# Kernel tuning notes

Measured on AMD Instinct MI355X. Metric: run time of the kernel, lower is better.

## Reference

```python
import jax, jax.numpy as jnp
import numpy as np

B, S, D = 1, 2048, 4096
HQ, HK, HD = 32, 8, 128


def setup_inputs() -> dict:
    key = jax.random.key(0)
    ks = jax.random.split(key, 6)
    x = jax.random.normal(ks[0], (B, S, D), jnp.float32) * 0.02
    wq = jax.random.normal(ks[1], (D, HQ * HD), jnp.float32) * 0.02
    wk = jax.random.normal(ks[2], (D, HK * HD), jnp.float32) * 0.02
    wv = jax.random.normal(ks[3], (D, HK * HD), jnp.float32) * 0.02
    wo = jax.random.normal(ks[4], (HQ * HD, D), jnp.float32) * 0.02
    # canonical RoPE frequencies: theta = 10000
    inv_freq = 1.0 / (10000.0 ** (jnp.arange(0, HD, 2, dtype=jnp.float32) / HD))  # [HD/2]
    t = jnp.arange(S, dtype=jnp.float32)
    ang = jnp.outer(t, inv_freq)  # [S, HD/2]
    return {
        "x": x,
        "freqs_cos": jnp.cos(ang),
        "freqs_sin": jnp.sin(ang),
        "wq": wq, "wk": wk, "wv": wv, "wo": wo,
    }


def _rope(t, cos, sin):
    # t: [B, S, H, HD]; pairs are consecutive elements (view_as_complex semantics)
    tr = t.reshape(*t.shape[:-1], HD // 2, 2)
    t0, t1 = tr[..., 0], tr[..., 1]
    c = cos[None, :, None, :]
    s = sin[None, :, None, :]
    o0 = t0 * c - t1 * s
    o1 = t0 * s + t1 * c
    return jnp.stack([o0, o1], axis=-1).reshape(t.shape)


def reference(x, freqs_cos, freqs_sin, wq, wk, wv, wo):
    b, s, _ = x.shape
    g = HQ // HK  # GQA group size
    xq = (x @ wq).reshape(b, s, HQ, HD)
    xk = (x @ wk).reshape(b, s, HK, HD)
    xv = (x @ wv).reshape(b, s, HK, HD)
    xq = _rope(xq, freqs_cos, freqs_sin)
    xk = _rope(xk, freqs_cos, freqs_sin)
    scale = 1.0 / jnp.sqrt(jnp.float32(HD))
    xqg = xq.reshape(b, s, HK, g, HD)
    # scores: [b, HK, g, s_q, s_k]
    scores = jnp.einsum("bqkgd,bnkd->bkgqn", xqg, xk) * scale
    causal = jnp.tril(jnp.ones((s, s), dtype=bool))
    scores = jnp.where(causal[None, None, None, :, :], scores, -jnp.inf)
    p = jax.nn.softmax(scores, axis=-1)
    out = jnp.einsum("bkgqn,bnkd->bqkgd", p, xv).reshape(b, s, HQ * HD)
    return out @ wo
```

## Files before the change

kernel.cpp:

```cpp
#include <hip/hip_runtime.h>
#include <stdint.h>

typedef __bf16 bf16_t;
typedef bf16_t bf16x8 __attribute__((ext_vector_type(8)));
typedef float f32x4 __attribute__((ext_vector_type(4)));
typedef unsigned int u32;
typedef unsigned short u16;

#define DEV_INLINE __device__ __forceinline__

#define S_LEN 2048
#define D_MODEL 4096
#define HQ 32
#define HK 8
#define HD 128
#define NQKV 6144

DEV_INLINE u16 f2bf(float x) {
  union { float f; uint32_t u; } v; v.f = x;
  uint32_t r = v.u + 0x7FFFu + ((v.u >> 16) & 1u);
  return (u16)(r >> 16);
}
DEV_INLINE float bf2f(u16 x) {
  union { uint32_t u; float f; } v; v.u = ((uint32_t)x) << 16;
  return v.f;
}
DEV_INLINE u32 pack2bf(float a, float b) {
  return (u32)f2bf(a) | ((u32)f2bf(b) << 16);
}

DEV_INLINE void async_load16(const void* g, void* l) {
  __builtin_amdgcn_global_load_lds(
      (const __attribute__((address_space(1))) u32*)g,
      (__attribute__((address_space(3))) u32*)l, 16, 0, 0);
}

DEV_INLINE f32x4 mfma16(bf16x8 a, bf16x8 b, f32x4 c) {
  return __builtin_amdgcn_mfma_f32_16x16x32_bf16(a, b, c, 0, 0, 0);
}

__global__ void cvt_f32_bf16(const float* __restrict__ in, u16* __restrict__ out, int n) {
  int i = (blockIdx.x * blockDim.x + threadIdx.x) * 4;
  if (i >= n) return;
  float4 v = *(const float4*)(in + i);
  union { u16 s[4]; uint2 u; } o;
  o.s[0] = f2bf(v.x); o.s[1] = f2bf(v.y); o.s[2] = f2bf(v.z); o.s[3] = f2bf(v.w);
  *(uint2*)(out + i) = o.u;
}

__global__ void transpose_f32_bf16(const float* __restrict__ in, u16* __restrict__ out,
                                   int R, int C) {
  __shared__ float tile[64][65];
  int tx = threadIdx.x, ty = threadIdx.y;
  int c0 = blockIdx.x * 64, r0 = blockIdx.y * 64;
#pragma unroll
  for (int i = 0; i < 16; ++i)
    tile[ty + i * 4][tx] = in[(long)(r0 + ty + i * 4) * C + c0 + tx];
  __syncthreads();
#pragma unroll
  for (int i = 0; i < 16; ++i)
    out[(long)(c0 + ty + i * 4) * R + r0 + tx] = f2bf(tile[tx][ty + i * 4]);
}

__global__ void transpose_bf16(const u16* __restrict__ in, u16* __restrict__ out,
                               int R, int C, int ld_in, int col_off) {
  __shared__ u16 tile[32][33];
  int tx = threadIdx.x, ty = threadIdx.y;
  int c0 = blockIdx.x * 32, r0 = blockIdx.y * 32;
#pragma unroll
  for (int i = 0; i < 4; ++i)
    tile[ty + i * 8][tx] = in[(long)(r0 + ty + i * 8) * ld_in + col_off + c0 + tx];
  __syncthreads();
#pragma unroll
  for (int i = 0; i < 4; ++i)
    out[(long)(c0 + ty + i * 8) * R + r0 + tx] = tile[tx][ty + i * 8];
}

__global__ void rope_bf16(const u16* __restrict__ in, const float* __restrict__ cosb,
                          const float* __restrict__ sinb, u16* __restrict__ out,
                          int H, int ld_in, int col_off, float scale) {
  int idx = blockIdx.x * blockDim.x + threadIdx.x;
  int j = idx & 63;
  int sh = idx >> 6;
  int s = sh / H, h = sh - s * H;
  const u16* ip = in + (long)s * ld_in + col_off + h * HD;
  union { u32 u; u16 s2[2]; } v; v.u = *(const u32*)(ip + 2 * j);
  float q0 = bf2f(v.s2[0]), q1 = bf2f(v.s2[1]);
  float c = cosb[s * 64 + j], sn = sinb[s * 64 + j];
  union { u16 s2[2]; u32 u; } o;
  o.s2[0] = f2bf((q0 * c - q1 * sn) * scale);
  o.s2[1] = f2bf((q0 * sn + q1 * c) * scale);
  *(u32*)(out + (long)sh * HD + 2 * j) = o.u;
}

#define BARRIER() asm volatile("s_barrier" ::: "memory")
#define WAIT_VM(N) asm volatile("s_waitcnt vmcnt(" #N ")" ::: "memory")

template <int BN, bool BF16OUT>
__global__ __launch_bounds__(256, 2) void gemm_db(
    const u16* __restrict__ A, const u16* __restrict__ Bt, void* __restrict__ Cv,
    int N, int K) {
  constexpr int NF = BN / 64;
  constexpr int BPT = (BN * 4) / 256;
  constexpr int LDSU = (128 + BN) * 32;

  __shared__ __attribute__((aligned(16))) u16 lds[2][LDSU];

  const int tid = threadIdx.x;
  const int lane = tid & 63, wave = tid >> 6;
  const int quad = lane >> 4, l15 = lane & 15;

  const int gx = gridDim.x;
  const int bid = blockIdx.y * gx + blockIdx.x;
  const int cpx = (gx * gridDim.y) >> 3;
  const int sw = (bid & 7) * cpx + (bid >> 3);
  const int bn = sw % gx, bm = sw / gx;

  const long arow = (long)bm * 128, brow = (long)bn * BN;
  const int NT = K >> 5;

  auto stage = [&](int ts) {
    const int k0 = ts * 32;
    u16* base = &lds[ts & 1][0];
#pragma unroll
    for (int j = 0; j < 2; ++j) {
      int c = tid + j * 256;
      int row = c >> 2, cc = c & 3, cs = cc ^ ((row >> 1) & 3);
      async_load16(A + (arow + row) * (long)K + k0 + cs * 8, base + c * 8);
    }
#pragma unroll
    for (int j = 0; j < BPT; ++j) {
      int c = tid + j * 256;
      int row = c >> 2, cc = c & 3, cs = cc ^ ((row >> 1) & 3);
      async_load16(Bt + (brow + row) * (long)K + k0 + cs * 8,
                   base + 4096 + c * 8);
    }
  };
  auto rdfrag = [&](const u16* base, int row) -> bf16x8 {
    return *(const bf16x8*)(base + row * 32 + ((quad ^ ((row >> 1) & 3)) * 8));
  };

  f32x4 acc[8][NF] = {};

  stage(0);
  WAIT_VM(0);
  BARRIER();

  for (int t = 0; t < NT; ++t) {
    if (t + 1 < NT) stage(t + 1);
    const u16* Ab = &lds[t & 1][0];
    const u16* Bb = Ab + 4096;
    bf16x8 bfr[NF];
#pragma unroll
    for (int j = 0; j < NF; ++j)
      bfr[j] = rdfrag(Bb, wave * (NF * 16) + j * 16 + l15);
    __builtin_amdgcn_s_setprio(1);
#pragma unroll
    for (int i = 0; i < 8; ++i) {
      bf16x8 af = rdfrag(Ab, i * 16 + l15);
#pragma unroll
      for (int j = 0; j < NF; ++j)
        acc[i][j] = mfma16(af, bfr[j], acc[i][j]);
    }
    __builtin_amdgcn_s_setprio(0);
    WAIT_VM(0);
    BARRIER();
  }

#pragma unroll
  for (int i = 0; i < 8; ++i) {
    const long row = (long)bm * 128 + i * 16 + quad * 4;
#pragma unroll
    for (int j = 0; j < NF; ++j) {
      const int col = bn * BN + wave * (NF * 16) + j * 16 + l15;
      if constexpr (BF16OUT) {
        u16* C = (u16*)Cv;
#pragma unroll
        for (int r = 0; r < 4; ++r) C[(row + r) * N + col] = f2bf(acc[i][j][r]);
      } else {
        float* C = (float*)Cv;
#pragma unroll
        for (int r = 0; r < 4; ++r) C[(row + r) * N + col] = acc[i][j][r];
      }
    }
  }
}

#define NEG_INF -1e30f
__global__ __launch_bounds__(256, 2) void attn_fwd(
    const u16* __restrict__ Qb, const u16* __restrict__ Kb,
    const u16* __restrict__ Vt, u16* __restrict__ Ob) {
  __shared__ __attribute__((aligned(16))) u16 Ks[2][64 * 128];
  __shared__ __attribute__((aligned(16))) u16 Vs[2][128 * 64];
  __shared__ __attribute__((aligned(16))) u16 Pts[4][16 * 64];
  const int tid = threadIdx.x;
  const int lane = tid & 63, wave = tid >> 6;
  const int quad = lane >> 4, l15 = lane & 15;
  const int lin = blockIdx.y * gridDim.x + blockIdx.x;
  const int h = lin & 31;
  const int pp = (lin >> 5) & 7;
  const int u = (lin >> 8) ? 15 - pp : pp;
  const int hk = h >> 2;
  const int swz = 2 * (l15 & 7);
  const int nt = 2 * (u + 1);

  bf16x8 qf[2][4];
#pragma unroll
  for (int n = 0; n < 2; ++n) {
    const u16* qrow = Qb + (long)(u * 128 + wave * 32 + n * 16 + l15) * (HQ * HD)
                      + h * HD + quad * 8;
#pragma unroll
    for (int ks = 0; ks < 4; ++ks) qf[n][ks] = *(const bf16x8*)(qrow + ks * 32);
  }

  auto stage = [&](int t) {
    const int b = t & 1;
#pragma unroll
    for (int it = 0; it < 4; ++it) {
      int c = tid + it * 256;
      int row = c >> 4, cc = c & 15, cs = cc ^ (row & 15);
      async_load16(Kb + (long)(t * 64 + row) * (HK * HD) + hk * HD + cs * 8,
                   (u16*)&Ks[b][0] + c * 8);
    }
#pragma unroll
    for (int it = 0; it < 4; ++it) {
      int c = tid + it * 256;
      int row = c >> 3, cc = c & 7, cs = cc ^ (row & 7);
      async_load16(Vt + (long)(hk * HD + row) * S_LEN + t * 64 + cs * 8,
                   (u16*)&Vs[b][0] + c * 8);
    }
  };

  float m_run[2] = {NEG_INF, NEG_INF}, l_run[2] = {0.f, 0.f};
  f32x4 oacc[8][2] = {};

  stage(0);
  __syncthreads();

  for (int t = 0; t < nt; ++t) {
    const int cur = t & 1;
    if (t + 1 < nt) stage(t + 1);

    if (t * 64 <= u * 128 + wave * 32 + 31) {
      f32x4 sc[4][2] = {};
      __builtin_amdgcn_s_setprio(1);
#pragma unroll
      for (int ks = 0; ks < 4; ++ks)
#pragma unroll
        for (int tj = 0; tj < 4; ++tj) {
          int row = tj * 16 + l15;
          bf16x8 kf = *(const bf16x8*)(&Ks[cur][0] + row * 128
                                       + (((ks * 4 + quad) ^ (row & 15)) * 8));
          sc[tj][0] = mfma16(kf, qf[0][ks], sc[tj][0]);
          sc[tj][1] = mfma16(kf, qf[1][ks], sc[tj][1]);
        }
      __builtin_amdgcn_s_setprio(0);

      const bool diag = (t >= 2 * u);
      const int kbase = t * 64 - u * 128;
#pragma unroll
      for (int n = 0; n < 2; ++n) {
        int qloc = wave * 32 + n * 16 + l15;
        if (diag) {
#pragma unroll
          for (int tj = 0; tj < 4; ++tj)
#pragma unroll
            for (int r = 0; r < 4; ++r)
              if (kbase + tj * 16 + quad * 4 + r > qloc) sc[tj][n][r] = NEG_INF;
        }
        float m = NEG_INF;
#pragma unroll
        for (int tj = 0; tj < 4; ++tj)
#pragma unroll
          for (int r = 0; r < 4; ++r) m = fmaxf(m, sc[tj][n][r]);
        m = fmaxf(m, __shfl_xor(m, 16));
        m = fmaxf(m, __shfl_xor(m, 32));
        if (!__all(m - m_run[n] <= 8.0f)) {
          float mnew = fmaxf(m_run[n], m);
          float alpha = __expf(m_run[n] - mnew);
          m_run[n] = mnew;
          l_run[n] *= alpha;
#pragma unroll
          for (int tj = 0; tj < 8; ++tj) oacc[tj][n] *= alpha;
        }
        float rs = 0.f;
#pragma unroll
        for (int tj = 0; tj < 4; ++tj)
#pragma unroll
          for (int r = 0; r < 4; ++r) {
            float p = __expf(sc[tj][n][r] - m_run[n]);
            sc[tj][n][r] = p;
            rs += p;
          }
        rs += __shfl_xor(rs, 16);
        rs += __shfl_xor(rs, 32);
        l_run[n] += rs;
      }

      u16* pw = &Pts[wave][0];
      bf16x8 pf0[2], pf1[2];
#pragma unroll
      for (int tj = 0; tj < 4; ++tj) {
        union { u32 w[2]; uint2 u2; } pk;
        pk.w[0] = pack2bf(sc[tj][0][0], sc[tj][0][1]);
        pk.w[1] = pack2bf(sc[tj][0][2], sc[tj][0][3]);
        *(uint2*)(pw + l15 * 64 + (((tj * 4 + quad) ^ swz) * 4)) = pk.u2;
      }
      __asm__ volatile("s_waitcnt lgkmcnt(0)" ::: "memory");
#pragma unroll
      for (int ks = 0; ks < 2; ++ks)
        pf0[ks] = *(const bf16x8*)(pw + l15 * 64 + (((ks * 8 + quad * 2) ^ swz) * 4));
      __asm__ volatile("s_waitcnt lgkmcnt(0)" ::: "memory");
#pragma unroll
      for (int tj = 0; tj < 4; ++tj) {
        union { u32 w[2]; uint2 u2; } pk;
        pk.w[0] = pack2bf(sc[tj][1][0], sc[tj][1][1]);
        pk.w[1] = pack2bf(sc[tj][1][2], sc[tj][1][3]);
        *(uint2*)(pw + l15 * 64 + (((tj * 4 + quad) ^ swz) * 4)) = pk.u2;
      }
      __asm__ volatile("s_waitcnt lgkmcnt(0)" ::: "memory");
#pragma unroll
      for (int ks = 0; ks < 2; ++ks)
        pf1[ks] = *(const bf16x8*)(pw + l15 * 64 + (((ks * 8 + quad * 2) ^ swz) * 4));

      __builtin_amdgcn_s_setprio(1);
#pragma unroll
      for (int ks = 0; ks < 2; ++ks)
#pragma unroll
        for (int tj = 0; tj < 8; ++tj) {
          int row = tj * 16 + l15;
          bf16x8 vf = *(const bf16x8*)(&Vs[cur][0] + row * 64
                                       + (((ks * 4 + quad) ^ (row & 7)) * 8));
          oacc[tj][0] = mfma16(vf, pf0[ks], oacc[tj][0]);
          oacc[tj][1] = mfma16(vf, pf1[ks], oacc[tj][1]);
        }
      __builtin_amdgcn_s_setprio(0);
    }

    __syncthreads();
  }

#pragma unroll
  for (int n = 0; n < 2; ++n) {
    float inv_l = 1.0f / l_run[n];
    long grow = u * 128 + wave * 32 + n * 16 + l15;
#pragma unroll
    for (int tj = 0; tj < 8; ++tj) {
      int gcol = h * HD + tj * 16 + quad * 4;
      union { u32 w[2]; uint2 u2; } pk;
      pk.w[0] = pack2bf(oacc[tj][n][0] * inv_l, oacc[tj][n][1] * inv_l);
      pk.w[1] = pack2bf(oacc[tj][n][2] * inv_l, oacc[tj][n][3] * inv_l);
      *(uint2*)(Ob + grow * (HQ * HD) + gcol) = pk.u2;
    }
  }
}

#define MB (1024L * 1024L)

extern "C" void kernel_launch(void* const* d_in, const int* in_sizes, int n_in,
                              void* d_out, int out_size, void* d_ws, size_t ws_size,
                              hipStream_t stream) {
  const float* x    = (const float*)d_in[0];
  const float* fcos = (const float*)d_in[1];
  const float* fsin = (const float*)d_in[2];
  const float* wq   = (const float*)d_in[3];
  const float* wk   = (const float*)d_in[4];
  const float* wv   = (const float*)d_in[5];
  const float* wo   = (const float*)d_in[6];
  float* out = (float*)d_out;

  char* ws = (char*)d_ws;
  u16* wt    = (u16*)(ws + 0 * MB);
  u16* xb    = (u16*)(ws + 48 * MB);
  u16* QKVb  = (u16*)(ws + 64 * MB);
  u16* Qb    = (u16*)(ws + 88 * MB);
  u16* Kb    = (u16*)(ws + 104 * MB);
  u16* Vt    = (u16*)(ws + 108 * MB);
  u16* attnb = (u16*)(ws + 112 * MB);

  const int M = S_LEN, D = D_MODEL;

  cvt_f32_bf16<<<(M * D) / 1024, 256, 0, stream>>>(x, xb, M * D);

  transpose_f32_bf16<<<dim3(D / 64, D / 64), dim3(64, 4), 0, stream>>>(wq, wt, D, HQ * HD);
  transpose_f32_bf16<<<dim3((HK * HD) / 64, D / 64), dim3(64, 4), 0, stream>>>(
      wk, wt + (long)(HQ * HD) * D, D, HK * HD);
  transpose_f32_bf16<<<dim3((HK * HD) / 64, D / 64), dim3(64, 4), 0, stream>>>(
      wv, wt + (long)(HQ * HD + HK * HD) * D, D, HK * HD);

  gemm_db<192, true><<<dim3(NQKV / 192, M / 128), 256, 0, stream>>>(
      xb, wt, QKVb, NQKV, D);

  rope_bf16<<<(M * HQ * 64) / 256, 256, 0, stream>>>(
      QKVb, fcos, fsin, Qb, HQ, NQKV, 0, 0.08838834764831845f);
  rope_bf16<<<(M * HK * 64) / 256, 256, 0, stream>>>(
      QKVb, fcos, fsin, Kb, HK, NQKV, HQ * HD, 1.0f);
  transpose_bf16<<<dim3((HK * HD) / 32, M / 32), dim3(32, 8), 0, stream>>>(
      QKVb, Vt, M, HK * HD, NQKV, HQ * HD + HK * HD);

  attn_fwd<<<dim3(16, HQ), 256, 0, stream>>>(Qb, Kb, Vt, attnb);

  transpose_f32_bf16<<<dim3(D / 64, D / 64), dim3(64, 4), 0, stream>>>(wo, wt, HQ * HD, D);
  gemm_db<128, false><<<dim3(D / 128, M / 128), 256, 0, stream>>>(
      attnb, wt, out, D, HQ * HD);
}
```

Measured before the change: 507.3 us.

## Replace double-buffered GEMM with 4-stage prefetching 512-thread GEMM

The GEMM becomes a 256-row tile computed by 512 threads in a 2D wave grid, with a 4-deep LDS ring buffer staged three tiles ahead. Register fragments are double-buffered so LDS reads for the next k-tile overlap the current MFMAs. The goal is to hide global-load latency and raise reuse per block. In exchange it needs much more LDS per block and more registers, and the fewer, larger blocks may reduce occupancy and tail balance.

```diff
diff --git a/kernel.cpp b/kernel.cpp
--- a/kernel.cpp
+++ b/kernel.cpp
@@ -96,19 +96,65 @@
 #define BARRIER() asm volatile("s_barrier" ::: "memory")
 #define WAIT_VM(N) asm volatile("s_waitcnt vmcnt(" #N ")" ::: "memory")
 
-template <int BN, bool BF16OUT>
-__global__ __launch_bounds__(256, 2) void gemm_db(
+#define VML() do { if constexpr (LPT == 4) { WAIT_VM(4); } else { WAIT_VM(3); } } while (0)
+
+#define KTILE(T, FAC, FAN, FBC, FBN, DO_READ, DO_STAGE, WMODE)            \
+  {                                                                       \
+    bf16x8 fbl[NF];                                                       \
+    if constexpr (!PFB) {                                                 \
+      const u16* Bb_ = &lds[(T) & 3][8192];                               \
+      _Pragma("unroll")                                                   \
+      for (int j = 0; j < NF; ++j)                                        \
+        fbl[j] = rdfrag(Bb_, wc * WCOLS + j * 16 + l15);                  \
+    }                                                                     \
+    if (DO_READ) {                                                        \
+      const u16* An_ = &lds[((T) + 1) & 3][0];                            \
+      _Pragma("unroll")                                                   \
+      for (int i = 0; i < MF; ++i)                                        \
+        FAN[i] = rdfrag(An_, wr * MROWS + i * 16 + l15);                  \
+      if constexpr (PFB) {                                                \
+        _Pragma("unroll")                                                 \
+        for (int j = 0; j < NF; ++j)                                      \
+          FBN[j] = rdfrag(An_ + 8192, wc * WCOLS + j * 16 + l15);         \
+      }                                                                   \
+    }                                                                     \
+    if (DO_STAGE) stageAB((T) + 3);                                       \
+    __builtin_amdgcn_s_setprio(1);                                        \
+    _Pragma("unroll")                                                     \
+    for (int i = 0; i < MF; ++i)                                          \
+      _Pragma("unroll")                                                   \
+      for (int j = 0; j < NF; ++j) {                                      \
+        if constexpr (PFB) acc[i][j] = mfma16(FAC[i], FBC[j], acc[i][j]); \
+        else               acc[i][j] = mfma16(FAC[i], fbl[j], acc[i][j]); \
+      }                                                                   \
+    __builtin_amdgcn_s_setprio(0);                                        \
+    if ((WMODE) == 0) { VML(); }                                          \
+    else if ((WMODE) == 1) { WAIT_VM(0); }                                \
+    BARRIER();                                                            \
+  }
+
+template <int BN, int WM, bool BF16OUT>
+__global__ __launch_bounds__(512, 2) void gemm_pf(
     const u16* __restrict__ A, const u16* __restrict__ Bt, void* __restrict__ Cv,
     int N, int K) {
-  constexpr int NF = BN / 64;
-  constexpr int BPT = (BN * 4) / 256;
-  constexpr int LDSU = (128 + BN) * 32;
-
-  __shared__ __attribute__((aligned(16))) u16 lds[2][LDSU];
+  constexpr int WN = 8 / WM;
+  constexpr int MROWS = 256 / WM;
+  constexpr int MF = MROWS / 16;
+  constexpr int NF = BN / (WN * 16);
+  constexpr int WCOLS = NF * 16;
+  constexpr int BCH = BN * 4;
+  constexpr int BISS = (BCH + 511) / 512;
+  constexpr int LPT = 2 + BISS;
+  constexpr bool PFB = (BN == 128);
+  constexpr int LDSU = (256 + BN) * 32;
+
+  __shared__ __attribute__((aligned(16))) u16 lds[4][LDSU];
 
   const int tid = threadIdx.x;
-  const int lane = tid & 63, wave = tid >> 6;
+  const int lane = tid & 63;
+  const int wave = tid >> 6;
   const int quad = lane >> 4, l15 = lane & 15;
+  const int wr = wave / WN, wc = wave % WN;
 
   const int gx = gridDim.x;
   const int bid = blockIdx.y * gx + blockIdx.x;
@@ -116,63 +162,66 @@
   const int sw = (bid & 7) * cpx + (bid >> 3);
   const int bn = sw % gx, bm = sw / gx;
 
-  const long arow = (long)bm * 128, brow = (long)bn * BN;
+  const long arow = (long)bm * 256, brow = (long)bn * BN;
   const int NT = K >> 5;
 
-  auto stage = [&](int ts) {
+  auto stageAB = [&](int ts) {
+    const int bs = ts & 3;
     const int k0 = ts * 32;
-    u16* base = &lds[ts & 1][0];
 #pragma unroll
     for (int j = 0; j < 2; ++j) {
-      int c = tid + j * 256;
+      int c = tid + j * 512;
       int row = c >> 2, cc = c & 3, cs = cc ^ ((row >> 1) & 3);
-      async_load16(A + (arow + row) * (long)K + k0 + cs * 8, base + c * 8);
-    }
-#pragma unroll
-    for (int j = 0; j < BPT; ++j) {
-      int c = tid + j * 256;
-      int row = c >> 2, cc = c & 3, cs = cc ^ ((row >> 1) & 3);
+      async_load16(A + (arow + row) * (long)K + k0 + cs * 8,
+                   (u16*)&lds[bs][0] + c * 8);
+    }
+#pragma unroll
+    for (int j = 0; j < BISS; ++j) {
+      int c = tid + j * 512;
+      int cd = (c < BCH) ? c : c - 256;
+      int row = cd >> 2, cc = cd & 3, cs = cc ^ ((row >> 1) & 3);
       async_load16(Bt + (brow + row) * (long)K + k0 + cs * 8,
-                   base + 4096 + c * 8);
+                   (u16*)&lds[bs][8192] + cd * 8);
     }
   };
   auto rdfrag = [&](const u16* base, int row) -> bf16x8 {
     return *(const bf16x8*)(base + row * 32 + ((quad ^ ((row >> 1) & 3)) * 8));
   };
 
-  f32x4 acc[8][NF] = {};
-
-  stage(0);
-  WAIT_VM(0);
+  f32x4 acc[MF][NF] = {};
+  bf16x8 fa0[MF], fa1[MF], fb0[NF], fb1[NF];
+
+  stageAB(0); stageAB(1); stageAB(2);
+  if constexpr (LPT == 4) { WAIT_VM(8); } else { WAIT_VM(6); }
   BARRIER();
-
-  for (int t = 0; t < NT; ++t) {
-    if (t + 1 < NT) stage(t + 1);
-    const u16* Ab = &lds[t & 1][0];
-    const u16* Bb = Ab + 4096;
-    bf16x8 bfr[NF];
-#pragma unroll
-    for (int j = 0; j < NF; ++j)
-      bfr[j] = rdfrag(Bb, wave * (NF * 16) + j * 16 + l15);
-    __builtin_amdgcn_s_setprio(1);
-#pragma unroll
-    for (int i = 0; i < 8; ++i) {
-      bf16x8 af = rdfrag(Ab, i * 16 + l15);
+  {
+    const u16* Ab_ = &lds[0][0];
+#pragma unroll
+    for (int i = 0; i < MF; ++i) fa0[i] = rdfrag(Ab_, wr * MROWS + i * 16 + l15);
+    if constexpr (PFB) {
 #pragma unroll
       for (int j = 0; j < NF; ++j)
-        acc[i][j] = mfma16(af, bfr[j], acc[i][j]);
-    }
-    __builtin_amdgcn_s_setprio(0);
-    WAIT_VM(0);
-    BARRIER();
-  }
-
-#pragma unroll
-  for (int i = 0; i < 8; ++i) {
-    const long row = (long)bm * 128 + i * 16 + quad * 4;
+        fb0[j] = rdfrag(Ab_ + 8192, wc * WCOLS + j * 16 + l15);
+    }
+  }
+
+  int t = 0;
+  for (; t < NT - 4; t += 2) {
+    KTILE(t,     fa0, fa1, fb0, fb1, true, true, 0);
+    KTILE(t + 1, fa1, fa0, fb1, fb0, true, true, 0);
+  }
+  KTILE(t,     fa0, fa1, fb0, fb1, true,  true,  0);
+  KTILE(t + 1, fa1, fa0, fb1, fb0, true,  false, 1);
+  KTILE(t + 2, fa0, fa1, fb0, fb1, true,  false, 2);
+  KTILE(t + 3, fa1, fa0, fb1, fb0, false, false, 2);
+  (void)t;
+
+#pragma unroll
+  for (int i = 0; i < MF; ++i) {
+    const long row = (long)bm * 256 + wr * MROWS + i * 16 + quad * 4;
 #pragma unroll
     for (int j = 0; j < NF; ++j) {
-      const int col = bn * BN + wave * (NF * 16) + j * 16 + l15;
+      const int col = bn * BN + wc * WCOLS + j * 16 + l15;
       if constexpr (BF16OUT) {
         u16* C = (u16*)Cv;
 #pragma unroll
@@ -388,7 +437,7 @@
   transpose_f32_bf16<<<dim3((HK * HD) / 64, D / 64), dim3(64, 4), 0, stream>>>(
       wv, wt + (long)(HQ * HD + HK * HD) * D, D, HK * HD);
 
-  gemm_db<192, true><<<dim3(NQKV / 192, M / 128), 256, 0, stream>>>(
+  gemm_pf<192, 2, true><<<dim3(NQKV / 192, M / 256), 512, 0, stream>>>(
       xb, wt, QKVb, NQKV, D);
 
   rope_bf16<<<(M * HQ * 64) / 256, 256, 0, stream>>>(
@@ -401,6 +450,6 @@
   attn_fwd<<<dim3(16, HQ), 256, 0, stream>>>(Qb, Kb, Vt, attnb);
 
   transpose_f32_bf16<<<dim3(D / 64, D / 64), dim3(64, 4), 0, stream>>>(wo, wt, HQ * HD, D);
-  gemm_db<128, false><<<dim3(D / 128, M / 128), 256, 0, stream>>>(
+  gemm_pf<128, 4, false><<<dim3(D / 128, M / 256), 512, 0, stream>>>(
       attnb, wt, out, D, HQ * HD);
 }
```

After: 483.4 us. 1.05x faster.
